# Kernel optimization log

Hardware: AMD Instinct MI355X
Metric: run time of the kernel (lower is better)

The kernel has to match this reference:

```python
import jax, jax.numpy as jnp
import numpy as np

VOCAB, EMB, H = 50000, 300, 64  # fgian_config: embed_dim=300, hidden_dim=64
POL = 3


def _lstm(x, lens, Wih, Whh, b):
    """Masked unidirectional LSTM (PyTorch gate order i,f,g,o).
    x: [B,T,D]; outputs zero past each sequence's length (packed-LSTM semantics)."""
    B, T, _ = x.shape
    Hh = Whh.shape[1]
    xs = jnp.einsum('btd,gd->btg', x, Wih) + b  # precompute input projection [B,T,4H]

    def step(carry, inp):
        h, c = carry
        xproj, t = inp
        g = xproj + h @ Whh.T
        i, f, gg, o = jnp.split(g, 4, axis=-1)
        i = jax.nn.sigmoid(i); f = jax.nn.sigmoid(f)
        gg = jnp.tanh(gg); o = jax.nn.sigmoid(o)
        c_new = f * c + i * gg
        h_new = o * jnp.tanh(c_new)
        m = (t < lens)[:, None]
        return (jnp.where(m, h_new, h), jnp.where(m, c_new, c)), jnp.where(m, h_new, 0.0)

    h0 = jnp.zeros((B, Hh), x.dtype)
    _, out = jax.lax.scan(step, (h0, h0), (xs.transpose(1, 0, 2), jnp.arange(T)))
    return out.transpose(1, 0, 2)


def _bilstm(x, lens, Wih_f, Whh_f, b_f, Wih_b, Whh_b, b_b):
    B, T, _ = x.shape
    t = jnp.arange(T)
    fwd = _lstm(x, lens, Wih_f, Whh_f, b_f)
    # reverse each sequence within its valid length, run fwd scan, reverse back
    ridx = jnp.clip(lens[:, None] - 1 - t[None, :], 0)  # [B,T]
    x_rev = jnp.take_along_axis(x, ridx[..., None], axis=1)
    bwd_rev = _lstm(x_rev, lens, Wih_b, Whh_b, b_b)
    bwd = jnp.take_along_axis(bwd_rev, ridx[..., None], axis=1)
    bwd = jnp.where((t[None, :] < lens[:, None])[..., None], bwd, 0.0)
    return jnp.concatenate([fwd, bwd], axis=-1)  # [B,T,2H]


def setup_inputs() -> dict:
    key = jax.random.key(0)
    ks = jax.random.split(key, 20)
    s = 0.1
    d = {
        'body_idx': jax.random.randint(ks[0], (128, 512), 0, VOCAB),
        'pun_idx': jax.random.randint(ks[1], (128, 256), 0, VOCAB),
        'emb': jax.random.normal(ks[2], (VOCAB, EMB), jnp.float32) * s,
        'w_u': jax.random.normal(ks[15], (6 * H,), jnp.float32) * s,
        'Wd': jax.random.normal(ks[16], (POL, 4 * H), jnp.float32) * s,
        'bd': jnp.zeros((POL,), jnp.float32),
    }
    names = ['bWih_f', 'bWhh_f', 'bb_f', 'bWih_b', 'bWhh_b', 'bb_b',
             'pWih_f', 'pWhh_f', 'pb_f', 'pWih_b', 'pWhh_b', 'pb_b']
    shapes = [(4 * H, EMB), (4 * H, H), (4 * H,)] * 4
    for i, (n, sh) in enumerate(zip(names, shapes)):
        d[n] = jax.random.normal(ks[3 + i], sh, jnp.float32) * s
    return d


def reference(body_idx, pun_idx, emb,
              bWih_f, bWhh_f, bb_f, bWih_b, bWhh_b, bb_b,
              pWih_f, pWhh_f, pb_f, pWih_b, pWhh_b, pb_b,
              w_u, Wd, bd):
    body_len = jnp.sum(body_idx != 0, axis=1)
    pun_len = jnp.sum(pun_idx != 0, axis=1)
    body_M = _bilstm(emb[body_idx], body_len, bWih_f, bWhh_f, bb_f, bWih_b, bWhh_b, bb_b)  # [B,T,2H]
    pun_M = _bilstm(emb[pun_idx], pun_len, pWih_f, pWhh_f, pb_f, pWih_b, pWhh_b, pb_b)     # [B,P,2H]

    # alignment[b,i,j] = [body_i, pun_j, body_i*pun_j] . w_u  -> fully vectorized
    w1, w2, w3 = jnp.split(w_u, 3)
    align = (jnp.einsum('btd,d->bt', body_M, w1)[:, :, None]
             + jnp.einsum('bpd,d->bp', pun_M, w2)[:, None, :]
             + jnp.einsum('btd,bpd->btp', body_M * w3, pun_M))  # [B,T,P]

    att_b = jax.nn.softmax(align.max(axis=2), axis=1)  # [B,T]
    f_pun2body = jnp.einsum('btd,bt->bd', body_M, att_b)
    att_p = jax.nn.softmax(align.max(axis=1), axis=1)  # [B,P]
    f_body2pun = jnp.einsum('bp,bpd->bd', att_p, pun_M)

    feat = jnp.concatenate([f_pun2body, f_body2pun], axis=1)  # [B,4H]
    return feat @ Wd.T + bd
```

## Files before the change

kernel.cpp:

```cpp
#include <hip/hip_runtime.h>


#define B 128
#define TBODY 512
#define TPUN 256
#define EMB 300
#define EMBP 320
#define VOCAB 50000
#define HID 64
#define G4 256
#define NG 512
#define DM 128

typedef __attribute__((ext_vector_type(8))) short bf16x8;
typedef __attribute__((ext_vector_type(4))) float floatx4;
typedef unsigned short u16;

#define OFF_XPB   0u
#define OFF_XPP   134217728u
#define OFF_BODYM 201326592u
#define OFF_PUNM  234881024u
#define OFF_SMALL 251658240u
#define OFF_ABODY (OFF_XPB + 0u)
#define OFF_APUN  (OFF_XPB + 262144u)
#define OFF_MT    (OFF_XPB + 393216u)
#define OFF_MP    (OFF_XPB + 655360u)
#define OFF_COLP  (OFF_XPB + 786432u)
#define OFF_EMBB  OFF_BODYM
#define OFF_WCB   OFF_PUNM
#define OFF_WCP   (OFF_PUNM + 327680u)
#define OFF_BIASB (OFF_PUNM + 655360u)
#define OFF_BIASP (OFF_PUNM + 657408u)
#define OFF_LENS  OFF_SMALL
#define OFF_FEAT  (OFF_SMALL + 1024u)

__device__ inline u16 f2bf(float v) {
    unsigned int u = __float_as_uint(v);
    unsigned int r = (u + 0x7FFFu + ((u >> 16) & 1u)) >> 16;
    return (u16)r;
}

__device__ inline void gload_lds16(const void* g, void* l) {
    __builtin_amdgcn_global_load_lds(
        (const __attribute__((address_space(1))) unsigned int*)g,
        (__attribute__((address_space(3))) unsigned int*)l, 16, 0, 0);
}

#define RL(v, k) __int_as_float(__builtin_amdgcn_readlane(__float_as_int(v), k))
#define SWZ(v, pat) __int_as_float(__builtin_amdgcn_ds_swizzle(__float_as_int(v), pat))

__global__ __launch_bounds__(256) void k_lens(const int* __restrict__ bidx,
                                              const int* __restrict__ pidx,
                                              int* __restrict__ lens) {
    int j = blockIdx.x, tid = threadIdx.x;
    const int* src; int n;
    if (j < B) { src = bidx + (size_t)j * TBODY; n = TBODY; }
    else       { src = pidx + (size_t)(j - B) * TPUN; n = TPUN; }
    int c = 0;
    for (int t = tid; t < n; t += 256) c += (src[t] != 0) ? 1 : 0;
    for (int o = 32; o; o >>= 1) c += __shfl_xor(c, o, 64);
    __shared__ int red[4];
    if ((tid & 63) == 0) red[tid >> 6] = c;
    __syncthreads();
    if (tid == 0) lens[j] = red[0] + red[1] + red[2] + red[3];
}

__global__ __launch_bounds__(256) void k_prep_emb(const float* __restrict__ emb,
                                                  u16* __restrict__ embb) {
    int e = blockIdx.x * 256 + threadIdx.x;
    int row = e / EMBP, d = e - row * EMBP;
    float v = (d < EMB) ? emb[(size_t)row * EMB + d] : 0.f;
    embb[e] = f2bf(v);
}

__global__ __launch_bounds__(256) void k_prep_w(
    const float* __restrict__ bWih_f, const float* __restrict__ bWih_b,
    const float* __restrict__ bb_f, const float* __restrict__ bb_b,
    const float* __restrict__ pWih_f, const float* __restrict__ pWih_b,
    const float* __restrict__ pb_f, const float* __restrict__ pb_b,
    u16* __restrict__ Wcb, u16* __restrict__ Wcp,
    float* __restrict__ biasb, float* __restrict__ biasp) {
    int e = blockIdx.x * 256 + threadIdx.x;
    const int WSZ = NG * EMBP;
    if (e < WSZ) {
        int g = e / EMBP, d = e - g * EMBP;
        float v = 0.f;
        if (d < EMB) v = (g < G4) ? bWih_f[g * EMB + d] : bWih_b[(g - G4) * EMB + d];
        Wcb[e] = f2bf(v);
    } else if (e < 2 * WSZ) {
        int ee = e - WSZ;
        int g = ee / EMBP, d = ee - g * EMBP;
        float v = 0.f;
        if (d < EMB) v = (g < G4) ? pWih_f[g * EMB + d] : pWih_b[(g - G4) * EMB + d];
        Wcp[ee] = f2bf(v);
    } else if (e < 2 * WSZ + NG) {
        int g = e - 2 * WSZ;
        biasb[g] = (g < G4) ? bb_f[g] : bb_b[g - G4];
    } else if (e < 2 * WSZ + 2 * NG) {
        int g = e - 2 * WSZ - NG;
        biasp[g] = (g < G4) ? pb_f[g] : pb_b[g - G4];
    }
}

__global__ __launch_bounds__(256) void k_gemm(const int* __restrict__ idx,
                                              const u16* __restrict__ embb,
                                              const u16* __restrict__ Wc,
                                              const float* __restrict__ biasc,
                                              float* __restrict__ out) {
    __shared__ u16 As[128 * 32];
    __shared__ u16 Bs[128 * 32];
    int tid = threadIdx.x, wave = tid >> 6, lane = tid & 63;
    int m0 = blockIdx.x * 128, g0 = blockIdx.y * 128;

    const u16* agp[2]; const u16* bgp[2];
    u16* asd[2]; u16* bsd[2];
#pragma unroll
    for (int j = 0; j < 2; j++) {
        int rbase = wave * 32 + j * 16;
        int r = rbase + (lane >> 2);
        int clog = (lane & 3) ^ (r & 3);
        int arow = idx[m0 + r];
        agp[j] = embb + (size_t)arow * EMBP + clog * 8;
        bgp[j] = Wc + (size_t)(g0 + r) * EMBP + clog * 8;
        asd[j] = As + rbase * 32;
        bsd[j] = Bs + rbase * 32;
    }

    int l15 = lane & 15, quad = lane >> 4;
    int mt0 = (wave >> 1) * 4, nt0 = (wave & 1) * 4;
    const u16* ard[4]; const u16* brd[4];
#pragma unroll
    for (int a = 0; a < 4; a++) {
        int r = (mt0 + a) * 16 + l15;
        ard[a] = As + r * 32 + ((quad ^ (r & 3)) * 8);
        int n = (nt0 + a) * 16 + l15;
        brd[a] = Bs + n * 32 + ((quad ^ (n & 3)) * 8);
    }

    floatx4 acc[4][4];
#pragma unroll
    for (int a = 0; a < 4; a++)
#pragma unroll
        for (int c = 0; c < 4; c++) acc[a][c] = (floatx4){0.f, 0.f, 0.f, 0.f};

    for (int k0 = 0; k0 < EMBP; k0 += 32) {
#pragma unroll
        for (int j = 0; j < 2; j++) {
            gload_lds16(agp[j] + k0, asd[j]);
            gload_lds16(bgp[j] + k0, bsd[j]);
        }
        __syncthreads();
        bf16x8 af[4], bfr[4];
#pragma unroll
        for (int a = 0; a < 4; a++) { af[a] = *(const bf16x8*)ard[a]; bfr[a] = *(const bf16x8*)brd[a]; }
#pragma unroll
        for (int a = 0; a < 4; a++)
#pragma unroll
            for (int c = 0; c < 4; c++)
                acc[a][c] = __builtin_amdgcn_mfma_f32_16x16x32_bf16(af[a], bfr[c], acc[a][c], 0, 0, 0);
        __syncthreads();
    }

#pragma unroll
    for (int c = 0; c < 4; c++) {
        int gcol = g0 + (nt0 + c) * 16 + l15;
        float bv = biasc[gcol];
#pragma unroll
        for (int a = 0; a < 4; a++) {
            int row0 = m0 + (mt0 + a) * 16 + quad * 4;
#pragma unroll
            for (int rg = 0; rg < 4; rg++)
                out[(size_t)(row0 + rg) * NG + gcol] = acc[a][c][rg] + bv;
        }
    }
}

#define DECLW(j) float Wk##j##0 = vw[4*j], Wk##j##1 = vw[4*j+1], \
                       Wk##j##2 = vw[4*j+2], Wk##j##3 = vw[4*j+3];
#define STEP4(j) \
    a0 = fmaf(RL(hq.x, j), Wk##j##0, a0); \
    a1 = fmaf(RL(hq.y, j), Wk##j##1, a1); \
    a2 = fmaf(RL(hq.z, j), Wk##j##2, a2); \
    a3 = fmaf(RL(hq.w, j), Wk##j##3, a3);

__global__ __launch_bounds__(256, 2) void k_scan(
    const float* __restrict__ xpB, const float* __restrict__ xpP,
    float* __restrict__ bodyM, float* __restrict__ punM,
    const int* __restrict__ lens,
    const float* __restrict__ bWhh_f, const float* __restrict__ bWhh_b,
    const float* __restrict__ pWhh_f, const float* __restrict__ pWhh_b) {
    int task = blockIdx.x, tid = threadIdx.x;
    int isPun = task >> 8;
    int sub = task & 255;
    int b = sub & 127, dir = sub >> 7;
    int T = isPun ? TPUN : TBODY;
    int len = lens[(isPun ? B : 0) + b];
    int w = tid >> 6, l = tid & 63;
    int g = l & 3, q = l >> 2;
    int u = w * 16 + q;
    const float* xp = (isPun ? xpP : xpB) + (size_t)b * T * NG + dir * G4;
    float* outp = (isPun ? punM : bodyM) + (size_t)b * T * DM + dir * HID;
    const float* Whh = isPun ? (dir ? pWhh_b : pWhh_f) : (dir ? bWhh_b : bWhh_f);

    const volatile float* vw = Whh + (size_t)(g * 64 + u) * 64;
    DECLW(0)  DECLW(1)  DECLW(2)  DECLW(3)
    DECLW(4)  DECLW(5)  DECLW(6)  DECLW(7)
    DECLW(8)  DECLW(9)  DECLW(10) DECLW(11)
    DECLW(12) DECLW(13) DECLW(14) DECLW(15)

    __shared__ __align__(16) float hbuf[2][64];
    if (tid < 64) hbuf[0][tid] = 0.f;
    __syncthreads();
    if (len <= 0) return;

    const float* xg = xp + g * 64 + u;
    float c = 0.f;
    float x_cur = xg[(size_t)(dir ? (len - 1) : 0) * NG];
    for (int s = 0; s < len; ++s) {
        int p = dir ? (len - 1 - s) : s;
        float xv = x_cur;
        int pn = dir ? (len - 2 - s) : (s + 1);
        pn = min(max(pn, 0), T - 1);
        x_cur = xg[(size_t)pn * NG];

        float4 hq = *(const float4*)(&hbuf[s & 1][(l & 15) * 4]);
        float a0 = xv, a1 = 0.f, a2 = 0.f, a3 = 0.f;
        STEP4(0)  STEP4(1)  STEP4(2)  STEP4(3)
        STEP4(4)  STEP4(5)  STEP4(6)  STEP4(7)
        STEP4(8)  STEP4(9)  STEP4(10) STEP4(11)
        STEP4(12) STEP4(13) STEP4(14) STEP4(15)
        float pre = (a0 + a1) + (a2 + a3);
        bool isg = (g == 2);
        float t_in = isg ? (2.f * pre) : (-pre);
        float e = __expf(t_in);
        float r = __builtin_amdgcn_rcpf(1.f + e);
        float val = isg ? fmaf(-2.f, r, 1.f) : r;
        float vi = SWZ(val, 0x8000);
        float vf = SWZ(val, 0x8055);
        float vg = SWZ(val, 0x80AA);
        float vo = SWZ(val, 0x80FF);
        c = fmaf(vf, c, vi * vg);
        float th = fmaf(-2.f, __builtin_amdgcn_rcpf(1.f + __expf(2.f * c)), 1.f);
        float h = vo * th;
        if (g == 0) {
            hbuf[(s & 1) ^ 1][u] = h;
            outp[(size_t)p * DM + u] = h;
        }
        __syncthreads();
    }
}

__global__ __launch_bounds__(256) void k_rowdot(const float* __restrict__ bodyM,
                                                const float* __restrict__ punM,
                                                const float* __restrict__ w_u,
                                                float* __restrict__ a_body,
                                                float* __restrict__ a_pun) {
    int wid = (blockIdx.x * 256 + threadIdx.x) >> 6;
    int lane = threadIdx.x & 63;
    const int NB = B * TBODY;
    const float* src; const float* wv; float* dst;
    if (wid < NB) { src = bodyM + (size_t)wid * DM; wv = w_u; dst = a_body + wid; }
    else { src = punM + (size_t)(wid - NB) * DM; wv = w_u + DM; dst = a_pun + (wid - NB); }
    float2 v = ((const float2*)src)[lane];
    float2 w = ((const float2*)wv)[lane];
    float s = v.x * w.x + v.y * w.y;
    for (int o = 32; o; o >>= 1) s += __shfl_xor(s, o, 64);
    if (lane == 0) *dst = s;
}

__global__ __launch_bounds__(256) void k_align(
    const float* __restrict__ bodyM, const float* __restrict__ punM,
    const float* __restrict__ a_body, const float* __restrict__ a_pun,
    const float* __restrict__ w_u,
    float* __restrict__ m_t, float* __restrict__ colpart) {
    __shared__ float bw[64 * 132];
    __shared__ float pu[64 * 129];
    __shared__ float colred[64 * 16];
    int tid = threadIdx.x;
    int tt = blockIdx.x, b = blockIdx.y;
    int t0 = tt * 64;
    int ti = tid >> 4, pi = tid & 15;
    const float* w3 = w_u + 2 * DM;
    const float* bsrc = bodyM + ((size_t)b * TBODY + t0) * DM;
#pragma unroll
    for (int j = 0; j < 8; j++) {
        int e = tid + 256 * j;
        int i = e >> 5, c4 = e & 31;
        float4 v = *(const float4*)(bsrc + i * DM + c4 * 4);
        float4 wv = *(const float4*)(w3 + c4 * 4);
        v.x *= wv.x; v.y *= wv.y; v.z *= wv.z; v.w *= wv.w;
        *(float4*)(bw + i * 132 + c4 * 4) = v;
    }
    float aB[4];
#pragma unroll
    for (int a = 0; a < 4; a++) aB[a] = a_body[(size_t)b * TBODY + t0 + ti * 4 + a];
    float mrun[4] = {-1e30f, -1e30f, -1e30f, -1e30f};
    for (int pc = 0; pc < 4; pc++) {
        __syncthreads();
        const float* psrc = punM + ((size_t)b * TPUN + pc * 64) * DM;
#pragma unroll
        for (int j = 0; j < 8; j++) {
            int e = tid + 256 * j;
            int i = e >> 5, c4 = e & 31;
            float4 v = *(const float4*)(psrc + i * DM + c4 * 4);
            pu[i * 129 + c4 * 4 + 0] = v.x;
            pu[i * 129 + c4 * 4 + 1] = v.y;
            pu[i * 129 + c4 * 4 + 2] = v.z;
            pu[i * 129 + c4 * 4 + 3] = v.w;
        }
        __syncthreads();
        float aP[4];
#pragma unroll
        for (int c = 0; c < 4; c++) aP[c] = a_pun[(size_t)b * TPUN + pc * 64 + pi * 4 + c];
        float C[4][4];
#pragma unroll
        for (int a = 0; a < 4; a++)
#pragma unroll
            for (int c = 0; c < 4; c++) C[a][c] = 0.f;
        for (int d4 = 0; d4 < 32; d4++) {
            float4 bq[4];
#pragma unroll
            for (int a = 0; a < 4; a++) bq[a] = *(const float4*)(bw + (ti * 4 + a) * 132 + d4 * 4);
#pragma unroll
            for (int dd = 0; dd < 4; dd++) {
                float pv[4];
#pragma unroll
                for (int c = 0; c < 4; c++) pv[c] = pu[(pi * 4 + c) * 129 + d4 * 4 + dd];
#pragma unroll
                for (int a = 0; a < 4; a++) {
                    float bvv = (dd == 0) ? bq[a].x : (dd == 1) ? bq[a].y : (dd == 2) ? bq[a].z : bq[a].w;
#pragma unroll
                    for (int c = 0; c < 4; c++) C[a][c] += bvv * pv[c];
                }
            }
        }
        float colv[4] = {-1e30f, -1e30f, -1e30f, -1e30f};
#pragma unroll
        for (int a = 0; a < 4; a++) {
            float rm = -1e30f;
#pragma unroll
            for (int c = 0; c < 4; c++) {
                float valv = C[a][c] + aB[a] + aP[c];
                rm = fmaxf(rm, valv);
                colv[c] = fmaxf(colv[c], valv);
            }
#pragma unroll
            for (int o = 1; o < 16; o <<= 1) rm = fmaxf(rm, __shfl_xor(rm, o, 64));
            mrun[a] = fmaxf(mrun[a], rm);
        }
#pragma unroll
        for (int c = 0; c < 4; c++) colred[(pi * 4 + c) * 16 + ti] = colv[c];
        __syncthreads();
        if (tid < 64) {
            float m = -1e30f;
#pragma unroll
            for (int k = 0; k < 16; k++) m = fmaxf(m, colred[tid * 16 + k]);
            colpart[((size_t)b * 8 + tt) * TPUN + pc * 64 + tid] = m;
        }
    }
    if (pi == 0) {
#pragma unroll
        for (int a = 0; a < 4; a++) m_t[(size_t)b * TBODY + t0 + ti * 4 + a] = mrun[a];
    }
}

__global__ __launch_bounds__(256) void k_colmax(const float* __restrict__ colpart,
                                                float* __restrict__ m_p) {
    int b = blockIdx.x, p = threadIdx.x;
    float m = -1e30f;
    for (int tt = 0; tt < 8; tt++) m = fmaxf(m, colpart[((size_t)b * 8 + tt) * TPUN + p]);
    m_p[(size_t)b * TPUN + p] = m;
}

__global__ __launch_bounds__(256) void k_feat(const float* __restrict__ bodyM,
                                              const float* __restrict__ punM,
                                              const float* __restrict__ m_t,
                                              const float* __restrict__ m_p,
                                              float* __restrict__ feat) {
    int bidx = blockIdx.x;
    int b = bidx & (B - 1), which = bidx >> 7;
    int n = which ? TPUN : TBODY;
    const float* sc = which ? (m_p + (size_t)b * TPUN) : (m_t + (size_t)b * TBODY);
    const float* src = which ? (punM + (size_t)b * TPUN * DM) : (bodyM + (size_t)b * TBODY * DM);
    float* dst = feat + (size_t)b * 256 + which * DM;
    int tid = threadIdx.x;
    __shared__ float e_lds[TBODY];
    __shared__ float red[8];
    __shared__ float red2[256];
    float mx = -1e30f;
    for (int t = tid; t < n; t += 256) mx = fmaxf(mx, sc[t]);
    for (int o = 32; o; o >>= 1) mx = fmaxf(mx, __shfl_xor(mx, o, 64));
    if ((tid & 63) == 0) red[tid >> 6] = mx;
    __syncthreads();
    mx = fmaxf(fmaxf(red[0], red[1]), fmaxf(red[2], red[3]));
    float se = 0.f;
    for (int t = tid; t < n; t += 256) {
        float ev = __expf(sc[t] - mx);
        e_lds[t] = ev;
        se += ev;
    }
    for (int o = 32; o; o >>= 1) se += __shfl_xor(se, o, 64);
    if ((tid & 63) == 0) red[4 + (tid >> 6)] = se;
    __syncthreads();
    se = red[4] + red[5] + red[6] + red[7];
    float inv = 1.f / se;
    int d = tid & 127, half = tid >> 7;
    float acc = 0.f;
    for (int t = half; t < n; t += 2) acc += e_lds[t] * src[(size_t)t * DM + d];
    red2[tid] = acc;
    __syncthreads();
    if (tid < DM) dst[tid] = (red2[tid] + red2[tid + 128]) * inv;
}

__global__ __launch_bounds__(256) void k_out(const float* __restrict__ feat,
                                             const float* __restrict__ Wd,
                                             const float* __restrict__ bd,
                                             float* __restrict__ outp) {
    int b = blockIdx.x, tid = threadIdx.x;
    float v = feat[(size_t)b * 256 + tid];
    __shared__ float red[12];
#pragma unroll
    for (int pol = 0; pol < 3; pol++) {
        float s = v * Wd[pol * 256 + tid];
        for (int o = 32; o; o >>= 1) s += __shfl_xor(s, o, 64);
        if ((tid & 63) == 0) red[pol * 4 + (tid >> 6)] = s;
    }
    __syncthreads();
    if (tid < 3) outp[b * 3 + tid] = red[tid * 4] + red[tid * 4 + 1] + red[tid * 4 + 2] + red[tid * 4 + 3] + bd[tid];
}

extern "C" void kernel_launch(void* const* d_in, const int* in_sizes, int n_in,
                              void* d_out, int out_size, void* d_ws, size_t ws_size,
                              hipStream_t stream) {
    const int* body_idx = (const int*)d_in[0];
    const int* pun_idx  = (const int*)d_in[1];
    const float* emb    = (const float*)d_in[2];
    const float* w_u    = (const float*)d_in[3];
    const float* Wd     = (const float*)d_in[4];
    const float* bd     = (const float*)d_in[5];
    const float* bWih_f = (const float*)d_in[6];
    const float* bWhh_f = (const float*)d_in[7];
    const float* bb_f   = (const float*)d_in[8];
    const float* bWih_b = (const float*)d_in[9];
    const float* bWhh_b = (const float*)d_in[10];
    const float* bb_b   = (const float*)d_in[11];
    const float* pWih_f = (const float*)d_in[12];
    const float* pWhh_f = (const float*)d_in[13];
    const float* pb_f   = (const float*)d_in[14];
    const float* pWih_b = (const float*)d_in[15];
    const float* pWhh_b = (const float*)d_in[16];
    const float* pb_b   = (const float*)d_in[17];

    char* ws = (char*)d_ws;
    float* xpB   = (float*)(ws + OFF_XPB);
    float* xpP   = (float*)(ws + OFF_XPP);
    float* bodyM = (float*)(ws + OFF_BODYM);
    float* punM  = (float*)(ws + OFF_PUNM);
    u16* embb    = (u16*)(ws + OFF_EMBB);
    u16* Wcb     = (u16*)(ws + OFF_WCB);
    u16* Wcp     = (u16*)(ws + OFF_WCP);
    float* biasb = (float*)(ws + OFF_BIASB);
    float* biasp = (float*)(ws + OFF_BIASP);
    int* lens    = (int*)(ws + OFF_LENS);
    float* a_body = (float*)(ws + OFF_ABODY);
    float* a_pun  = (float*)(ws + OFF_APUN);
    float* m_t    = (float*)(ws + OFF_MT);
    float* m_p    = (float*)(ws + OFF_MP);
    float* colpart = (float*)(ws + OFF_COLP);
    float* feat   = (float*)(ws + OFF_FEAT);
    float* outp   = (float*)d_out;

    k_lens<<<dim3(256), dim3(256), 0, stream>>>(body_idx, pun_idx, lens);
    k_prep_emb<<<dim3(62500), dim3(256), 0, stream>>>(emb, embb);
    k_prep_w<<<dim3(1284), dim3(256), 0, stream>>>(bWih_f, bWih_b, bb_f, bb_b,
                                                   pWih_f, pWih_b, pb_f, pb_b,
                                                   Wcb, Wcp, biasb, biasp);
    k_gemm<<<dim3(512, 4), dim3(256), 0, stream>>>(body_idx, embb, Wcb, biasb, xpB);
    k_gemm<<<dim3(256, 4), dim3(256), 0, stream>>>(pun_idx, embb, Wcp, biasp, xpP);
    hipMemsetAsync(ws + OFF_BODYM, 0, (size_t)(33554432u + 16777216u), stream);
    k_scan<<<dim3(512), dim3(256), 0, stream>>>(xpB, xpP, bodyM, punM, lens,
                                                bWhh_f, bWhh_b, pWhh_f, pWhh_b);
    k_rowdot<<<dim3(24576), dim3(256), 0, stream>>>(bodyM, punM, w_u, a_body, a_pun);
    k_align<<<dim3(8, 128), dim3(256), 0, stream>>>(bodyM, punM, a_body, a_pun, w_u, m_t, colpart);
    k_colmax<<<dim3(128), dim3(256), 0, stream>>>(colpart, m_p);
    k_feat<<<dim3(256), dim3(256), 0, stream>>>(bodyM, punM, m_t, m_p, feat);
    k_out<<<dim3(128), dim3(256), 0, stream>>>(feat, Wd, bd, outp);
}
```

Before: 718.8 us.

## Split LSTM recurrent matvec over two wave groups with LDS partial-sum reduction

The scan kernel now uses 512 threads per block. The 64-wide hidden reduction is split in half across two groups of four waves, each holding only 32 weights, and the second group's partial sums are passed through shared memory. This halves the serial FMA chain per step, which is the latency-critical path of the recurrence. In exchange it adds an extra __syncthreads and an LDS round trip per timestep. The gate broadcast also changes from ds_swizzle to DPP quad-permute, which avoids the LDS pipe.

```diff
diff --git a/kernel.cpp b/kernel.cpp
--- a/kernel.cpp
+++ b/kernel.cpp
@@ -47,7 +47,8 @@
 }
 
 #define RL(v, k) __int_as_float(__builtin_amdgcn_readlane(__float_as_int(v), k))
-#define SWZ(v, pat) __int_as_float(__builtin_amdgcn_ds_swizzle(__float_as_int(v), pat))
+#define QBC(v, gg) __int_as_float(__builtin_amdgcn_update_dpp( \
+    0, __float_as_int(v), (gg) * 0x55, 0xF, 0xF, true))
 
 __global__ __launch_bounds__(256) void k_lens(const int* __restrict__ bidx,
                                               const int* __restrict__ pidx,
@@ -177,13 +178,14 @@
 
 #define DECLW(j) float Wk##j##0 = vw[4*j], Wk##j##1 = vw[4*j+1], \
                        Wk##j##2 = vw[4*j+2], Wk##j##3 = vw[4*j+3];
-#define STEP4(j) \
-    a0 = fmaf(RL(hq.x, j), Wk##j##0, a0); \
-    a1 = fmaf(RL(hq.y, j), Wk##j##1, a1); \
-    a2 = fmaf(RL(hq.z, j), Wk##j##2, a2); \
-    a3 = fmaf(RL(hq.w, j), Wk##j##3, a3);
-
-__global__ __launch_bounds__(256, 2) void k_scan(
+#define STEP4H(jj) \
+    a0 = fmaf(RL(hq.x, j0 + jj), Wk##jj##0, a0); \
+    a1 = fmaf(RL(hq.y, j0 + jj), Wk##jj##1, a1); \
+    a2 = fmaf(RL(hq.z, j0 + jj), Wk##jj##2, a2); \
+    a3 = fmaf(RL(hq.w, j0 + jj), Wk##jj##3, a3);
+
+__global__ __attribute__((amdgpu_flat_work_group_size(512, 512),
+                          amdgpu_waves_per_eu(4, 4))) void k_scan(
     const float* __restrict__ xpB, const float* __restrict__ xpP,
     float* __restrict__ bodyM, float* __restrict__ punM,
     const int* __restrict__ lens,
@@ -195,56 +197,63 @@
     int b = sub & 127, dir = sub >> 7;
     int T = isPun ? TPUN : TBODY;
     int len = lens[(isPun ? B : 0) + b];
-    int w = tid >> 6, l = tid & 63;
+    int wv = tid >> 6, l = tid & 63;
+    int kh = wv >> 2;
+    int ug = wv & 3;
     int g = l & 3, q = l >> 2;
-    int u = w * 16 + q;
+    int u = ug * 16 + q;
     const float* xp = (isPun ? xpP : xpB) + (size_t)b * T * NG + dir * G4;
     float* outp = (isPun ? punM : bodyM) + (size_t)b * T * DM + dir * HID;
     const float* Whh = isPun ? (dir ? pWhh_b : pWhh_f) : (dir ? bWhh_b : bWhh_f);
 
-    const volatile float* vw = Whh + (size_t)(g * 64 + u) * 64;
-    DECLW(0)  DECLW(1)  DECLW(2)  DECLW(3)
-    DECLW(4)  DECLW(5)  DECLW(6)  DECLW(7)
-    DECLW(8)  DECLW(9)  DECLW(10) DECLW(11)
-    DECLW(12) DECLW(13) DECLW(14) DECLW(15)
+    const volatile float* vw = Whh + (size_t)(g * 64 + u) * 64 + kh * 32;
+    DECLW(0) DECLW(1) DECLW(2) DECLW(3)
+    DECLW(4) DECLW(5) DECLW(6) DECLW(7)
 
     __shared__ __align__(16) float hbuf[2][64];
+    __shared__ float part[256];
     if (tid < 64) hbuf[0][tid] = 0.f;
     __syncthreads();
     if (len <= 0) return;
 
+    int j0 = kh * 8;
     const float* xg = xp + g * 64 + u;
     float c = 0.f;
-    float x_cur = xg[(size_t)(dir ? (len - 1) : 0) * NG];
+    float x_cur = 0.f;
+    if (!kh) x_cur = xg[(size_t)(dir ? (len - 1) : 0) * NG];
     for (int s = 0; s < len; ++s) {
         int p = dir ? (len - 1 - s) : s;
         float xv = x_cur;
-        int pn = dir ? (len - 2 - s) : (s + 1);
-        pn = min(max(pn, 0), T - 1);
-        x_cur = xg[(size_t)pn * NG];
-
+        if (!kh) {
+            int pn = dir ? (len - 2 - s) : (s + 1);
+            pn = min(max(pn, 0), T - 1);
+            x_cur = xg[(size_t)pn * NG];
+        }
         float4 hq = *(const float4*)(&hbuf[s & 1][(l & 15) * 4]);
         float a0 = xv, a1 = 0.f, a2 = 0.f, a3 = 0.f;
-        STEP4(0)  STEP4(1)  STEP4(2)  STEP4(3)
-        STEP4(4)  STEP4(5)  STEP4(6)  STEP4(7)
-        STEP4(8)  STEP4(9)  STEP4(10) STEP4(11)
-        STEP4(12) STEP4(13) STEP4(14) STEP4(15)
+        STEP4H(0) STEP4H(1) STEP4H(2) STEP4H(3)
+        STEP4H(4) STEP4H(5) STEP4H(6) STEP4H(7)
         float pre = (a0 + a1) + (a2 + a3);
-        bool isg = (g == 2);
-        float t_in = isg ? (2.f * pre) : (-pre);
-        float e = __expf(t_in);
-        float r = __builtin_amdgcn_rcpf(1.f + e);
-        float val = isg ? fmaf(-2.f, r, 1.f) : r;
-        float vi = SWZ(val, 0x8000);
-        float vf = SWZ(val, 0x8055);
-        float vg = SWZ(val, 0x80AA);
-        float vo = SWZ(val, 0x80FF);
-        c = fmaf(vf, c, vi * vg);
-        float th = fmaf(-2.f, __builtin_amdgcn_rcpf(1.f + __expf(2.f * c)), 1.f);
-        float h = vo * th;
-        if (g == 0) {
-            hbuf[(s & 1) ^ 1][u] = h;
-            outp[(size_t)p * DM + u] = h;
+        if (kh) part[ug * 64 + l] = pre;
+        __syncthreads();
+        if (!kh) {
+            pre += part[ug * 64 + l];
+            bool isg = (g == 2);
+            float t_in = isg ? (2.f * pre) : (-pre);
+            float e = __expf(t_in);
+            float r = __builtin_amdgcn_rcpf(1.f + e);
+            float val = isg ? fmaf(-2.f, r, 1.f) : r;
+            float vi = QBC(val, 0);
+            float vf = QBC(val, 1);
+            float vg = QBC(val, 2);
+            float vo = QBC(val, 3);
+            c = fmaf(vf, c, vi * vg);
+            float th = fmaf(-2.f, __builtin_amdgcn_rcpf(1.f + __expf(2.f * c)), 1.f);
+            float h = vo * th;
+            if (g == 0) {
+                hbuf[(s & 1) ^ 1][u] = h;
+                outp[(size_t)p * DM + u] = h;
+            }
         }
         __syncthreads();
     }
@@ -478,7 +487,7 @@
     k_gemm<<<dim3(512, 4), dim3(256), 0, stream>>>(body_idx, embb, Wcb, biasb, xpB);
     k_gemm<<<dim3(256, 4), dim3(256), 0, stream>>>(pun_idx, embb, Wcp, biasp, xpP);
     hipMemsetAsync(ws + OFF_BODYM, 0, (size_t)(33554432u + 16777216u), stream);
-    k_scan<<<dim3(512), dim3(256), 0, stream>>>(xpB, xpP, bodyM, punM, lens,
+    k_scan<<<dim3(512), dim3(512), 0, stream>>>(xpB, xpP, bodyM, punM, lens,
                                                 bWhh_f, bWhh_b, pWhh_f, pWhh_b);
     k_rowdot<<<dim3(24576), dim3(256), 0, stream>>>(bodyM, punM, w_u, a_body, a_pun);
     k_align<<<dim3(8, 128), dim3(256), 0, stream>>>(bodyM, punM, a_body, a_pun, w_u, m_t, colpart);
```

Result: slower. 838.3 us (+16.6%).
